# Optimization experiments

Hardware: AMD Instinct MI355X
Metric: run time of the kernel (lower is better)

Reference implementation:

```python
import jax, jax.numpy as jnp
import numpy as np
from math import pi as PI

N = 50000       # nodes
E = 625000      # edges
G = 64          # graphs in batch
H = 128         # hidden_channels
FLT = 128       # num_filters
NG = 50         # num_gaussians
L = 6           # num_layers
CUTOFF = 10.0
LOG2 = float(np.log(2.0))


def ssp(x):
    # ShiftedSoftplus
    return jax.nn.softplus(x) - LOG2


def setup_inputs() -> dict:
    key = jax.random.key(0)
    ks = jax.random.split(key, 20)
    xav = lambda k, shp: jax.random.normal(k, shp, jnp.float32) * jnp.sqrt(2.0 / (shp[-2] + shp[-1]))
    inp = {
        "z": jax.random.randint(ks[0], (N,), 0, 100),
        "pos": jax.random.normal(ks[1], (N, 3), jnp.float32),
        "batch": jnp.sort(jax.random.randint(ks[2], (N,), 0, G)),
        "edge_index": jax.random.randint(ks[3], (2, E), 0, N),
        "emb_table": jax.random.normal(ks[4], (100, H), jnp.float32),
        # per-layer stacked params, Linear stored as (in, out)
        "lin_W": xav(ks[5], (L, H, FLT)),
        "mlp_W1": xav(ks[6], (L, NG, FLT)),
        "mlp_b1": jnp.zeros((L, FLT), jnp.float32),
        "mlp_W2": xav(ks[7], (L, FLT, FLT)),
        "mlp_b2": jnp.zeros((L, FLT), jnp.float32),
        "v_W1": xav(ks[8], (L, FLT, H)),
        "v_b1": jnp.zeros((L, H), jnp.float32),
        "v_W2": xav(ks[9], (L, H, H)),
        "v_b2": jnp.zeros((L, H), jnp.float32),
        "u_W1": xav(ks[10], (H, H // 2)),
        "u_b1": jnp.zeros((H // 2,), jnp.float32),
        "u_W2": xav(ks[11], (H // 2, 1)),
        "u_b2": jnp.zeros((1,), jnp.float32),
    }
    return inp


def reference(z, pos, batch, edge_index, emb_table, lin_W, mlp_W1, mlp_b1,
              mlp_W2, mlp_b2, v_W1, v_b1, v_W2, v_b2, u_W1, u_b1, u_W2, u_b2):
    row, col = edge_index[0], edge_index[1]  # (j, i)
    dist = jnp.linalg.norm(pos[row] - pos[col], axis=-1)  # [E]

    # gaussian distance embedding
    offset = jnp.linspace(0.0, CUTOFF, NG)
    coeff = -0.5 / (offset[1] - offset[0]) ** 2
    dist_emb = jnp.exp(coeff * (dist[:, None] - offset[None, :]) ** 2)  # [E, NG]

    # cosine cutoff
    C = 0.5 * (jnp.cos(dist * (PI / CUTOFF)) + 1.0)  # [E]

    v = emb_table[z]  # [N, H]
    for l in range(L):
        # update_e
        W = ssp(dist_emb @ mlp_W1[l] + mlp_b1[l]) @ mlp_W2[l] + mlp_b2[l]
        W = W * C[:, None]                       # [E, F]
        e = (v @ lin_W[l])[row] * W              # gather v[j], filter multiply
        # update_v
        agg = jax.ops.segment_sum(e, col, num_segments=N)  # scatter-add to i
        out = ssp(agg @ v_W1[l] + v_b1[l]) @ v_W2[l] + v_b2[l]
        v = v + out

    # update_u readout
    h = ssp(v @ u_W1 + u_b1) @ u_W2 + u_b2       # [N, 1]
    u = jax.ops.segment_sum(h, batch, num_segments=G)  # [G, 1]
    return u
```

## Files before the change

kernel.cpp:

```cpp
#include <hip/hip_runtime.h>
#include <math.h>

#define H 128
#define NG 50
#define TB 2048
#define DMAX 12.0f
#define LOG2F_ 0.69314718055994531f

typedef __attribute__((ext_vector_type(8))) short bfrag8;
typedef __attribute__((ext_vector_type(4))) float f32x4;
typedef __attribute__((ext_vector_type(8))) unsigned short u16x8;

__device__ __forceinline__ float sspf(float x) {
    float xc = fminf(x, 60.f);
    float r = __logf(1.f + __expf(xc)) - LOG2F_;
    return r + fmaxf(x - 60.f, 0.f);
}
__device__ __forceinline__ float bf2f(unsigned short u) {
    union { unsigned int i; float f; } c; c.i = ((unsigned int)u) << 16; return c.f;
}
__device__ __forceinline__ unsigned short f2bf(float f) {
    union { float f; unsigned int i; } c; c.f = f;
    unsigned int r = c.i + 0x7fffu + ((c.i >> 16) & 1u);
    return (unsigned short)(r >> 16);
}

__global__ void prep_w_kernel(const float* __restrict__ linW, const float* __restrict__ vW1,
                              const float* __restrict__ vW2, unsigned short* __restrict__ Wt) {
    int mat = blockIdx.x >> 4;
    int local = (blockIdx.x & 15) * 256 + threadIdx.x;
    int nrow = local >> 5;
    int k4 = local & 31;
    const float* src = (mat < 6) ? linW + mat * 16384
                     : (mat < 12) ? vW1 + (mat - 6) * 16384
                                  : vW2 + (mat - 12) * 16384;
    ushort4 o;
    o.x = f2bf(src[(k4 * 4 + 0) * H + nrow]);
    o.y = f2bf(src[(k4 * 4 + 1) * H + nrow]);
    o.z = f2bf(src[(k4 * 4 + 2) * H + nrow]);
    o.w = f2bf(src[(k4 * 4 + 3) * H + nrow]);
    *(ushort4*)(Wt + mat * 16384 + nrow * H + k4 * 4) = o;
}

__global__ void prep_u_kernel(const float* __restrict__ uW1, unsigned short* __restrict__ Ut) {
    int idx = blockIdx.x * 256 + threadIdx.x;
    int c = idx >> 7, k = idx & 127;
    Ut[c * H + k] = f2bf(uW1[k * 64 + c]);
}

__global__ void edge_dist_kernel(const int* __restrict__ ei, const float* __restrict__ pos,
                                 float* __restrict__ et, int* __restrict__ deg,
                                 int E_, float inv_step) {
    int e = blockIdx.x * 256 + threadIdx.x;
    if (e >= E_) return;
    int j = ei[e];
    int i = ei[E_ + e];
    float dx = pos[j*3+0] - pos[i*3+0];
    float dy = pos[j*3+1] - pos[i*3+1];
    float dz = pos[j*3+2] - pos[i*3+2];
    float d = sqrtf(dx*dx + dy*dy + dz*dz);
    float t = d * inv_step;
    t = fminf(t, (float)(TB - 2) + 0.9999f);
    et[e] = t;
    atomicAdd(&deg[i], 1);
}

__global__ void hist_pb_kernel(const int* __restrict__ deg, int* __restrict__ bhist,
                               int* __restrict__ lrank, int n, int nb) {
    __shared__ int h[64];
    const int tid = threadIdx.x;
    if (tid < 64) h[tid] = 0;
    __syncthreads();
    int i = blockIdx.x * 256 + tid;
    if (i < n) lrank[i] = atomicAdd(&h[min(deg[i], 63)], 1);
    __syncthreads();
    if (tid < 64) bhist[tid * nb + blockIdx.x] = h[tid];
}

__global__ void scanb_kernel(int* __restrict__ bhist, int* __restrict__ base, int nb) {
    const int b = threadIdx.x;
    int run = 0;
    for (int k0 = 0; k0 < nb; k0 += 8) {
        int v[8];
        #pragma unroll
        for (int u = 0; u < 8; ++u)
            v[u] = (k0 + u < nb) ? bhist[b * nb + k0 + u] : 0;
        #pragma unroll
        for (int u = 0; u < 8; ++u) {
            int t = v[u];
            if (k0 + u < nb) bhist[b * nb + k0 + u] = run;
            run += t;
        }
    }
    int incl = run;
    #pragma unroll
    for (int off = 1; off < 64; off <<= 1) {
        int y = __shfl_up(incl, off, 64);
        if (b >= off) incl += y;
    }
    int total = __shfl(incl, 63, 64);
    base[b] = total - incl;
}

__global__ void place_kernel(const int* __restrict__ deg, const int* __restrict__ bhist,
                             const int* __restrict__ base, const int* __restrict__ lrank,
                             int* __restrict__ perm, int* __restrict__ iperm,
                             int* __restrict__ sdeg, int n, int nb) {
    int i = blockIdx.x * 256 + threadIdx.x;
    if (i >= n) return;
    int d = deg[i];
    int b = min(d, 63);
    int pos = base[b] + bhist[b * nb + blockIdx.x] + lrank[i];
    perm[pos] = i;
    iperm[i] = pos;
    sdeg[pos] = d;
}

__global__ void scanA_kernel(const int* __restrict__ sdeg, int* __restrict__ bsum, int n) {
    __shared__ int ws[16];
    int tid = threadIdx.x;
    int idx = blockIdx.x * 1024 + tid;
    int x = (idx < n) ? sdeg[idx] : 0;
    #pragma unroll
    for (int off = 32; off > 0; off >>= 1) x += __shfl_xor(x, off, 64);
    int lane = tid & 63, wid = tid >> 6;
    if (lane == 0) ws[wid] = x;
    __syncthreads();
    if (tid == 0) {
        int s = 0;
        #pragma unroll
        for (int i = 0; i < 16; ++i) s += ws[i];
        bsum[blockIdx.x] = s;
    }
}

__global__ void scanC_kernel(const int* __restrict__ sdeg, const int* __restrict__ bsum,
                             int* __restrict__ row_ptr, int* __restrict__ cursor, int n) {
    __shared__ int wsum[16];
    __shared__ int boff_s;
    int tid = threadIdx.x;
    int idx = blockIdx.x * 1024 + tid;
    int lane = tid & 63, wid = tid >> 6;
    if (tid == 0) {
        int s = 0;
        for (int b = 0; b < (int)blockIdx.x; ++b) s += bsum[b];
        boff_s = s;
    }
    int x = (idx < n) ? sdeg[idx] : 0;
    int v = x;
    #pragma unroll
    for (int off = 1; off < 64; off <<= 1) {
        int y = __shfl_up(v, off, 64);
        if (lane >= off) v += y;
    }
    if (lane == 63) wsum[wid] = v;
    __syncthreads();
    int woff = 0;
    for (int w = 0; w < wid; ++w) woff += wsum[w];
    int excl = boff_s + woff + v - x;
    if (idx < n) { row_ptr[idx] = excl; cursor[idx] = excl; }
    if (idx == n - 1) row_ptr[n] = excl + x;
}

__global__ void csr_fill_kernel(const int* __restrict__ ei, const float* __restrict__ et,
                                const int* __restrict__ iperm,
                                int* __restrict__ cursor, int* __restrict__ esrc,
                                float* __restrict__ et2, int E_) {
    int e = blockIdx.x * 256 + threadIdx.x;
    if (e >= E_) return;
    int pi = iperm[ei[E_ + e]];
    int slot = atomicAdd(&cursor[pi], 1);
    esrc[slot] = iperm[ei[e]];
    et2[slot] = et[e];
}

__global__ __launch_bounds__(256) void table_all_kernel(
        const float* __restrict__ mW1, const float* __restrict__ mb1,
        const float* __restrict__ mW2, const float* __restrict__ mb2,
        unsigned short* __restrict__ tbl, float step) {
    __shared__ float gs[32][52];
    __shared__ float h1s[32][132];
    const int l = blockIdx.x >> 6;
    const int r0 = (blockIdx.x & 63) * 32;
    const float* W1 = mW1 + l * NG * H;
    const float* b1 = mb1 + l * H;
    const float* W2 = mW2 + l * H * H;
    const float* b2 = mb2 + l * H;
    const int tid = threadIdx.x;
    const float offstep = 10.0f / 49.0f;
    const float coeff = -0.5f / (offstep * offstep);

    for (int idx = tid; idx < 32 * NG; idx += 256) {
        int r = idx / NG, q = idx - r * NG;
        float dd = (r0 + r) * step - q * offstep;
        gs[r][q] = __expf(coeff * dd * dd);
    }
    __syncthreads();

    const int c = tid & 127, rb = (tid >> 7) * 16;
    {
        float acc[16];
        float bv = b1[c];
        #pragma unroll
        for (int r = 0; r < 16; ++r) acc[r] = bv;
        for (int q = 0; q < NG; ++q) {
            float w = W1[q * H + c];
            #pragma unroll
            for (int r = 0; r < 16; ++r) acc[r] = fmaf(gs[rb + r][q], w, acc[r]);
        }
        #pragma unroll
        for (int r = 0; r < 16; ++r) h1s[rb + r][c] = sspf(acc[r]);
    }
    __syncthreads();
    {
        float acc[16];
        float bv = b2[c];
        #pragma unroll
        for (int r = 0; r < 16; ++r) acc[r] = bv;
        for (int f4 = 0; f4 < 32; ++f4) {
            float w0 = W2[(f4 * 4 + 0) * H + c];
            float w1 = W2[(f4 * 4 + 1) * H + c];
            float w2 = W2[(f4 * 4 + 2) * H + c];
            float w3 = W2[(f4 * 4 + 3) * H + c];
            #pragma unroll
            for (int r = 0; r < 16; ++r) {
                float4 h = *(const float4*)&h1s[rb + r][f4 * 4];
                acc[r] = fmaf(h.x, w0, acc[r]);
                acc[r] = fmaf(h.y, w1, acc[r]);
                acc[r] = fmaf(h.z, w2, acc[r]);
                acc[r] = fmaf(h.w, w3, acc[r]);
            }
        }
        #pragma unroll
        for (int r = 0; r < 16; ++r) {
            float d = (r0 + rb + r) * step;
            float C = 0.5f * (cosf(d * 0.31415926535897932f) + 1.0f);
            tbl[(size_t)l * TB * H + (size_t)(r0 + rb + r) * H + c] = f2bf(acc[r] * C);
        }
    }
}

__global__ __launch_bounds__(256) void gemm_rs_embed_kernel(
        const int* __restrict__ z, const int* __restrict__ perm,
        const float* __restrict__ emb, const unsigned short* __restrict__ Wt,
        unsigned short* __restrict__ vbf, unsigned short* __restrict__ outB, int n) {
    __shared__ unsigned short t1s[4 * 16 * H];
    const int tid = threadIdx.x;
    const int task = blockIdx.x * 4 + (tid >> 6);
    const int lane = tid & 63, l16 = lane & 15, quad = lane >> 4;
    char* t1w = (char*)(t1s + (tid >> 6) * (16 * H));
    const size_t r0 = (size_t)task * 16;
    const int p = (int)r0 + l16;
    if (p >= n) return;

    const float* erow = emb + (size_t)z[perm[p]] * H;
    bfrag8 af[4];
    #pragma unroll
    for (int kc = 0; kc < 4; ++kc) {
        const int c0 = (kc * 4 + quad) * 8;
        float4 a = *(const float4*)(erow + c0);
        float4 b = *(const float4*)(erow + c0 + 4);
        u16x8 o;
        o[0] = f2bf(a.x); o[1] = f2bf(a.y); o[2] = f2bf(a.z); o[3] = f2bf(a.w);
        o[4] = f2bf(b.x); o[5] = f2bf(b.y); o[6] = f2bf(b.z); o[7] = f2bf(b.w);
        *(u16x8*)(vbf + (size_t)p * H + c0) = o;
        af[kc] = (bfrag8)o;
    }

    #pragma unroll
    for (int ch = 0; ch < 2; ++ch) {
        bfrag8 bf[4][4];
        f32x4 acc[4];
        #pragma unroll
        for (int nt = 0; nt < 4; ++nt) {
            #pragma unroll
            for (int kc = 0; kc < 4; ++kc)
                bf[nt][kc] = *(const bfrag8*)(Wt + (size_t)(ch * 64 + nt * 16 + l16) * H
                                              + (kc * 4 + quad) * 8);
            acc[nt] = (f32x4){0.f, 0.f, 0.f, 0.f};
        }
        #pragma unroll
        for (int nt = 0; nt < 4; ++nt)
            #pragma unroll
            for (int kc = 0; kc < 4; ++kc)
                acc[nt] = __builtin_amdgcn_mfma_f32_16x16x32_bf16(af[kc], bf[nt][kc],
                                                                  acc[nt], 0, 0, 0);
        #pragma unroll
        for (int nt = 0; nt < 4; ++nt) {
            const int col = ch * 64 + nt * 16 + l16;
            const int chunk = col >> 3;
            #pragma unroll
            for (int reg = 0; reg < 4; ++reg) {
                int m = quad * 4 + reg;
                *(unsigned short*)(t1w + m * 256 + ((chunk ^ m) * 16) + (col & 7) * 2)
                    = f2bf(acc[nt][reg]);
            }
        }
    }
    asm volatile("s_waitcnt lgkmcnt(0)" ::: "memory");
    {
        const int m = lane >> 2, cg = lane & 3;
        const size_t gr = r0 + m;
        #pragma unroll
        for (int c4 = 0; c4 < 4; ++c4) {
            int chunk = cg * 4 + c4;
            u16x8 d8 = *(const u16x8*)(t1w + m * 256 + ((chunk ^ m) * 16));
            *(u16x8*)(outB + gr * H + cg * 32 + c4 * 8) = d8;
        }
    }
}

__global__ __launch_bounds__(256, 4) void layer_kernel(
        const int* __restrict__ row_ptr, const int* __restrict__ esrc,
        const float* __restrict__ et, const unsigned short* __restrict__ tbl,
        const unsigned short* __restrict__ vlin,
        const unsigned short* __restrict__ W1t, const unsigned short* __restrict__ W2t,
        const unsigned short* __restrict__ W3t,
        const float* __restrict__ b1, const float* __restrict__ b2,
        unsigned short* __restrict__ vbf, unsigned short* __restrict__ outNext, int n) {
    __shared__ unsigned short bufA[16 * H];
    __shared__ unsigned short bufB[16 * H];
    const int tid = threadIdx.x;
    const int w = tid >> 6, lane = tid & 63;
    const int r0 = blockIdx.x * 16;
    const int l16 = lane & 15, quad = lane >> 4;

    const int rrow = tid >> 4, rcolg = tid & 15;
    const int rnode = r0 + rrow;
    u16x8 rv = {0,0,0,0,0,0,0,0};
    if (rnode < n) rv = *(const u16x8*)(vbf + (size_t)rnode * H + rcolg * 8);

    {
        const int nd = w * 4 + (lane >> 4);
        const int sub = lane & 15;
        const int node = r0 + nd;
        float acc[8] = {0.f, 0.f, 0.f, 0.f, 0.f, 0.f, 0.f, 0.f};
        if (node < n) {
            const int s = row_ptr[node], e_end = row_ptr[node + 1];
            int k = s;
            for (; k + 4 <= e_end; k += 4) {
                u16x8 w0[4], w1[4], vj[4];
                float fr[4];
                #pragma unroll
                for (int e = 0; e < 4; ++e) {
                    int j = esrc[k + e];
                    float t = et[k + e];
                    int i0 = (int)t;
                    fr[e] = t - (float)i0;
                    w0[e] = *(const u16x8*)(tbl + (size_t)i0 * H + sub * 8);
                    w1[e] = *(const u16x8*)(tbl + (size_t)i0 * H + H + sub * 8);
                    vj[e] = *(const u16x8*)(vlin + (size_t)j * H + sub * 8);
                }
                #pragma unroll
                for (int e = 0; e < 4; ++e)
                    #pragma unroll
                    for (int c = 0; c < 8; ++c) {
                        float a = bf2f(w0[e][c]);
                        acc[c] = fmaf(bf2f(vj[e][c]), fmaf(bf2f(w1[e][c]) - a, fr[e], a), acc[c]);
                    }
            }
            for (; k < e_end; ++k) {
                int j = esrc[k];
                float t = et[k];
                int i0 = (int)t;
                float fr = t - (float)i0;
                u16x8 w0v = *(const u16x8*)(tbl + (size_t)i0 * H + sub * 8);
                u16x8 w1v = *(const u16x8*)(tbl + (size_t)i0 * H + H + sub * 8);
                u16x8 vj  = *(const u16x8*)(vlin + (size_t)j * H + sub * 8);
                #pragma unroll
                for (int c = 0; c < 8; ++c) {
                    float a = bf2f(w0v[c]);
                    acc[c] = fmaf(bf2f(vj[c]), fmaf(bf2f(w1v[c]) - a, fr, a), acc[c]);
                }
            }
        }
        u16x8 o;
        #pragma unroll
        for (int c = 0; c < 8; ++c) o[c] = f2bf(acc[c]);
        *(u16x8*)((char*)bufA + nd * 256 + ((sub ^ nd) * 16)) = o;
    }
    __syncthreads();

    {
        bfrag8 af[4];
        #pragma unroll
        for (int kc = 0; kc < 4; ++kc)
            af[kc] = *(const bfrag8*)((char*)bufA + l16 * 256 + (((kc * 4 + quad) ^ l16) * 16));
        #pragma unroll
        for (int nt2 = 0; nt2 < 2; ++nt2) {
            const int colt = w * 32 + nt2 * 16;
            bfrag8 bf[4];
            #pragma unroll
            for (int kc = 0; kc < 4; ++kc)
                bf[kc] = *(const bfrag8*)(W1t + (size_t)(colt + l16) * H + (kc * 4 + quad) * 8);
            f32x4 acc = (f32x4){0.f, 0.f, 0.f, 0.f};
            #pragma unroll
            for (int kc = 0; kc < 4; ++kc)
                acc = __builtin_amdgcn_mfma_f32_16x16x32_bf16(af[kc], bf[kc], acc, 0, 0, 0);
            const int f = colt + l16;
            const float bv = b1[f];
            const int chunk = f >> 3;
            #pragma unroll
            for (int reg = 0; reg < 4; ++reg) {
                int mr = quad * 4 + reg;
                *(unsigned short*)((char*)bufB + mr * 256 + ((chunk ^ mr) * 16) + (f & 7) * 2)
                    = f2bf(sspf(acc[reg] + bv));
            }
        }
    }
    __syncthreads();

    {
        bfrag8 af[4];
        #pragma unroll
        for (int kc = 0; kc < 4; ++kc)
            af[kc] = *(const bfrag8*)((char*)bufB + l16 * 256 + (((kc * 4 + quad) ^ l16) * 16));
        #pragma unroll
        for (int nt2 = 0; nt2 < 2; ++nt2) {
            const int colt = w * 32 + nt2 * 16;
            bfrag8 bf[4];
            #pragma unroll
            for (int kc = 0; kc < 4; ++kc)
                bf[kc] = *(const bfrag8*)(W2t + (size_t)(colt + l16) * H + (kc * 4 + quad) * 8);
            f32x4 acc = (f32x4){0.f, 0.f, 0.f, 0.f};
            #pragma unroll
            for (int kc = 0; kc < 4; ++kc)
                acc = __builtin_amdgcn_mfma_f32_16x16x32_bf16(af[kc], bf[kc], acc, 0, 0, 0);
            const int col = colt + l16;
            const float bv = b2[col];
            const int chunk = col >> 3;
            #pragma unroll
            for (int reg = 0; reg < 4; ++reg) {
                int mr = quad * 4 + reg;
                *(unsigned short*)((char*)bufA + mr * 256 + ((chunk ^ mr) * 16) + (col & 7) * 2)
                    = f2bf(acc[reg] + bv);
            }
        }
    }
    __syncthreads();

    {
        u16x8 d8 = *(const u16x8*)((char*)bufA + rrow * 256 + ((rcolg ^ rrow) * 16));
        u16x8 ob;
        #pragma unroll
        for (int c = 0; c < 8; ++c) ob[c] = f2bf(bf2f(rv[c]) + bf2f(d8[c]));
        if (rnode < n) *(u16x8*)(vbf + (size_t)rnode * H + rcolg * 8) = ob;
        *(u16x8*)((char*)bufB + rrow * 256 + ((rcolg ^ rrow) * 16)) = ob;
    }
    if (!W3t) return;
    __syncthreads();

    {
        bfrag8 af[4];
        #pragma unroll
        for (int kc = 0; kc < 4; ++kc)
            af[kc] = *(const bfrag8*)((char*)bufB + l16 * 256 + (((kc * 4 + quad) ^ l16) * 16));
        #pragma unroll
        for (int nt2 = 0; nt2 < 2; ++nt2) {
            const int colt = w * 32 + nt2 * 16;
            bfrag8 bf[4];
            #pragma unroll
            for (int kc = 0; kc < 4; ++kc)
                bf[kc] = *(const bfrag8*)(W3t + (size_t)(colt + l16) * H + (kc * 4 + quad) * 8);
            f32x4 acc = (f32x4){0.f, 0.f, 0.f, 0.f};
            #pragma unroll
            for (int kc = 0; kc < 4; ++kc)
                acc = __builtin_amdgcn_mfma_f32_16x16x32_bf16(af[kc], bf[kc], acc, 0, 0, 0);
            const int col = colt + l16;
            const int chunk = col >> 3;
            #pragma unroll
            for (int reg = 0; reg < 4; ++reg) {
                int mr = quad * 4 + reg;
                *(unsigned short*)((char*)bufA + mr * 256 + ((chunk ^ mr) * 16) + (col & 7) * 2)
                    = f2bf(acc[reg]);
            }
        }
    }
    __syncthreads();
    {
        u16x8 d8 = *(const u16x8*)((char*)bufA + rrow * 256 + ((rcolg ^ rrow) * 16));
        if (rnode < n) *(u16x8*)(outNext + (size_t)rnode * H + rcolg * 8) = d8;
    }
}

__global__ __launch_bounds__(256) void readout1_kernel(
        const unsigned short* __restrict__ vbf, const unsigned short* __restrict__ Ut,
        const float* __restrict__ b1, const float* __restrict__ W2,
        const float* __restrict__ b2, const int* __restrict__ batch,
        const int* __restrict__ perm, float* __restrict__ partial, int n) {
    __shared__ unsigned short As[64 * H];
    __shared__ unsigned short Bs[64 * H];
    __shared__ float gbin[64];
    const int tid = threadIdx.x;
    const int row0 = blockIdx.x * 64;

    #pragma unroll
    for (int it = 0; it < 4; ++it) {
        int idx = it * 256 + tid;
        int r = idx >> 4, c = idx & 15;
        int gr = row0 + r;
        float4 val = (gr < n) ? *(const float4*)(vbf + (size_t)gr * H + c * 8)
                              : make_float4(0.f, 0.f, 0.f, 0.f);
        *(float4*)((char*)As + r * 256 + ((c ^ (r & 15)) * 16)) = val;
    }
    #pragma unroll
    for (int it = 0; it < 4; ++it) {
        int idx = it * 256 + tid;
        int r = idx >> 4, c = idx & 15;
        float4 val = *(const float4*)(Ut + r * H + c * 8);
        *(float4*)((char*)Bs + r * 256 + ((c ^ (r & 15)) * 16)) = val;
    }
    if (tid < 64) gbin[tid] = 0.f;
    __syncthreads();

    const int lane = tid & 63, w = tid >> 6;
    const int l16 = lane & 15, quad = lane >> 4;
    const int rA = w * 16 + l16;

    bfrag8 af[4];
    #pragma unroll
    for (int kc = 0; kc < 4; ++kc) {
        int c = kc * 4 + quad;
        af[kc] = *(const bfrag8*)((const char*)As + rA * 256 + ((c ^ (rA & 15)) * 16));
    }
    f32x4 acc[4];
    #pragma unroll
    for (int nt = 0; nt < 4; ++nt) acc[nt] = (f32x4){0.f, 0.f, 0.f, 0.f};
    #pragma unroll
    for (int nt = 0; nt < 4; ++nt) {
        const int rB = nt * 16 + l16;
        #pragma unroll
        for (int kc = 0; kc < 4; ++kc) {
            int c = kc * 4 + quad;
            bfrag8 bfr = *(const bfrag8*)((const char*)Bs + rB * 256 + ((c ^ (rB & 15)) * 16));
            acc[nt] = __builtin_amdgcn_mfma_f32_16x16x32_bf16(af[kc], bfr, acc[nt], 0, 0, 0);
        }
    }

    const float b2v = b2[0];
    float rowsum[4];
    #pragma unroll
    for (int reg = 0; reg < 4; ++reg) {
        float s = 0.f;
        #pragma unroll
        for (int nt = 0; nt < 4; ++nt) {
            int col = nt * 16 + l16;
            s += sspf(acc[nt][reg] + b1[col]) * W2[col];
        }
        s += __shfl_xor(s, 1, 64);
        s += __shfl_xor(s, 2, 64);
        s += __shfl_xor(s, 4, 64);
        s += __shfl_xor(s, 8, 64);
        rowsum[reg] = s;
    }
    if (l16 == 0) {
        #pragma unroll
        for (int reg = 0; reg < 4; ++reg) {
            int node = row0 + w * 16 + quad * 4 + reg;
            if (node < n) atomicAdd(&gbin[batch[perm[node]]], rowsum[reg] + b2v);
        }
    }
    __syncthreads();
    if (tid < 64) partial[blockIdx.x * 64 + tid] = gbin[tid];
}

__global__ void readout2_kernel(const float* __restrict__ partial, float* __restrict__ out,
                                int nb) {
    __shared__ float red[256];
    const int tid = threadIdx.x;
    const int g = tid & 63, q = tid >> 6;
    float acc = 0.f;
    for (int b = q; b < nb; b += 4) acc += partial[b * 64 + g];
    red[tid] = acc;
    __syncthreads();
    if (tid < 64) out[tid] = red[tid] + red[tid + 64] + red[tid + 128] + red[tid + 192];
}

extern "C" void kernel_launch(void* const* d_in, const int* in_sizes, int n_in,
                              void* d_out, int out_size, void* d_ws, size_t ws_size,
                              hipStream_t stream) {
    const int*   z       = (const int*)d_in[0];
    const float* pos     = (const float*)d_in[1];
    const int*   batch   = (const int*)d_in[2];
    const int*   ei      = (const int*)d_in[3];
    const float* emb     = (const float*)d_in[4];
    const float* lin_W   = (const float*)d_in[5];
    const float* mlp_W1  = (const float*)d_in[6];
    const float* mlp_b1  = (const float*)d_in[7];
    const float* mlp_W2  = (const float*)d_in[8];
    const float* mlp_b2  = (const float*)d_in[9];
    const float* v_W1    = (const float*)d_in[10];
    const float* v_b1    = (const float*)d_in[11];
    const float* v_W2    = (const float*)d_in[12];
    const float* v_b2    = (const float*)d_in[13];
    const float* u_W1    = (const float*)d_in[14];
    const float* u_b1    = (const float*)d_in[15];
    const float* u_W2    = (const float*)d_in[16];
    const float* u_b2    = (const float*)d_in[17];
    const int n  = in_sizes[0];
    const int E_ = in_sizes[3] / 2;
    float* out = (float*)d_out;

    char* wp = (char*)d_ws;
    auto alloc = [&](size_t bytes) { char* p = wp; wp += (bytes + 255) & ~(size_t)255; return p; };
    const int GB = (n + 63) / 64;
    const int NB1K = (n + 1023) / 1024;
    const int NB256 = (n + 255) / 256;
    unsigned short* vbf     = (unsigned short*)alloc((size_t)n * H * 2);
    unsigned short* vlinA   = (unsigned short*)alloc((size_t)n * H * 2);
    unsigned short* vlinB   = (unsigned short*)alloc((size_t)n * H * 2);
    unsigned short* WtAll   = (unsigned short*)alloc((size_t)18 * H * H * 2);
    unsigned short* Ut      = (unsigned short*)alloc((size_t)64 * H * 2);
    unsigned short* tbl     = (unsigned short*)alloc((size_t)6 * TB * H * 2);
    float* et      = (float*)alloc((size_t)E_ * 4);
    float* et2     = (float*)alloc((size_t)E_ * 4);
    int*   esrc    = (int*)alloc((size_t)E_ * 4);
    int*   deg     = (int*)alloc((size_t)n * 4);
    int*   sdeg    = (int*)alloc((size_t)n * 4);
    int*   perm    = (int*)alloc((size_t)n * 4);
    int*   iperm   = (int*)alloc((size_t)n * 4);
    int*   lrank   = (int*)alloc((size_t)n * 4);
    int*   row_ptr = (int*)alloc((size_t)(n + 1) * 4);
    int*   cursor  = (int*)alloc((size_t)n * 4);
    int*   bsum    = (int*)alloc((size_t)NB1K * 4);
    int*   bhist   = (int*)alloc((size_t)64 * NB256 * 4);
    int*   base    = (int*)alloc(64 * 4);
    float* partial = (float*)alloc((size_t)GB * 64 * 4);

    const float step = DMAX / TB;
    hipMemsetAsync(deg, 0, (size_t)n * 4, stream);

    prep_w_kernel<<<288, 256, 0, stream>>>(lin_W, v_W1, v_W2, WtAll);
    prep_u_kernel<<<32, 256, 0, stream>>>(u_W1, Ut);
    table_all_kernel<<<384, 256, 0, stream>>>(mlp_W1, mlp_b1, mlp_W2, mlp_b2, tbl, step);
    edge_dist_kernel<<<(E_ + 255) / 256, 256, 0, stream>>>(ei, pos, et, deg, E_, 1.0f / step);
    hist_pb_kernel<<<NB256, 256, 0, stream>>>(deg, bhist, lrank, n, NB256);
    scanb_kernel<<<1, 64, 0, stream>>>(bhist, base, NB256);
    place_kernel<<<NB256, 256, 0, stream>>>(deg, bhist, base, lrank, perm, iperm, sdeg, n, NB256);
    scanA_kernel<<<NB1K, 1024, 0, stream>>>(sdeg, bsum, n);
    scanC_kernel<<<NB1K, 1024, 0, stream>>>(sdeg, bsum, row_ptr, cursor, n);
    csr_fill_kernel<<<(E_ + 255) / 256, 256, 0, stream>>>(ei, et, iperm, cursor, esrc, et2, E_);

    const int nchunk = (n + 15) / 16;
    const int GRS = (nchunk + 3) / 4;
    gemm_rs_embed_kernel<<<GRS, 256, 0, stream>>>(z, perm, emb, WtAll, vbf, vlinA, n);
    unsigned short* cur = vlinA;
    unsigned short* nxt = vlinB;
    for (int l = 0; l < 6; ++l) {
        const unsigned short* W3t = (l < 5) ? (WtAll + (l + 1) * H * H) : nullptr;
        layer_kernel<<<nchunk, 256, 0, stream>>>(row_ptr, esrc, et2,
                                                 tbl + (size_t)l * TB * H, cur,
                                                 WtAll + (6 + l) * H * H,
                                                 WtAll + (12 + l) * H * H, W3t,
                                                 v_b1 + l * H, v_b2 + l * H,
                                                 vbf, nxt, n);
        unsigned short* tmp = cur; cur = nxt; nxt = tmp;
    }
    readout1_kernel<<<GB, 256, 0, stream>>>(vbf, Ut, u_b1, u_W2, u_b2, batch, perm, partial, n);
    readout2_kernel<<<1, 256, 0, stream>>>(partial, out, GB);
}
```

Before: 662.8 us.

## Use nearest-bin filter table, pack edge data, fuse readout into last layer

Doubles the filter table resolution and replaces linear interpolation with a nearest-bin lookup. Each edge now loads one table row instead of two, with no interpolation FMAs. Edge source and bin index are packed into one int2 array, and the gather loop is unrolled to 8 edges to expose more outstanding loads. The readout MLP and per-graph partial sums are fused into the final layer kernel, which removes a separate launch and a reread of node features. The cost is a nearest-bin approximation in place of interpolation, a larger table to build, and a larger readout2 reduction.

```diff
diff --git a/kernel.cpp b/kernel.cpp
--- a/kernel.cpp
+++ b/kernel.cpp
@@ -3,7 +3,7 @@
 
 #define H 128
 #define NG 50
-#define TB 2048
+#define TB 4096
 #define DMAX 12.0f
 #define LOG2F_ 0.69314718055994531f
 
@@ -49,7 +49,7 @@
 }
 
 __global__ void edge_dist_kernel(const int* __restrict__ ei, const float* __restrict__ pos,
-                                 float* __restrict__ et, int* __restrict__ deg,
+                                 int* __restrict__ eint, int* __restrict__ deg,
                                  int E_, float inv_step) {
     int e = blockIdx.x * 256 + threadIdx.x;
     if (e >= E_) return;
@@ -59,9 +59,8 @@
     float dy = pos[j*3+1] - pos[i*3+1];
     float dz = pos[j*3+2] - pos[i*3+2];
     float d = sqrtf(dx*dx + dy*dy + dz*dz);
-    float t = d * inv_step;
-    t = fminf(t, (float)(TB - 2) + 0.9999f);
-    et[e] = t;
+    int ir = (int)(d * inv_step + 0.5f);
+    eint[e] = min(ir, TB - 1);
     atomicAdd(&deg[i], 1);
 }
 
@@ -162,16 +161,14 @@
     if (idx == n - 1) row_ptr[n] = excl + x;
 }
 
-__global__ void csr_fill_kernel(const int* __restrict__ ei, const float* __restrict__ et,
+__global__ void csr_fill_kernel(const int* __restrict__ ei, const int* __restrict__ eint,
                                 const int* __restrict__ iperm,
-                                int* __restrict__ cursor, int* __restrict__ esrc,
-                                float* __restrict__ et2, int E_) {
+                                int* __restrict__ cursor, int2* __restrict__ epack, int E_) {
     int e = blockIdx.x * 256 + threadIdx.x;
     if (e >= E_) return;
     int pi = iperm[ei[E_ + e]];
     int slot = atomicAdd(&cursor[pi], 1);
-    esrc[slot] = iperm[ei[e]];
-    et2[slot] = et[e];
+    epack[slot] = make_int2(iperm[ei[e]], eint[e]);
 }
 
 __global__ __launch_bounds__(256) void table_all_kernel(
@@ -180,8 +177,8 @@
         unsigned short* __restrict__ tbl, float step) {
     __shared__ float gs[32][52];
     __shared__ float h1s[32][132];
-    const int l = blockIdx.x >> 6;
-    const int r0 = (blockIdx.x & 63) * 32;
+    const int l = blockIdx.x >> 7;
+    const int r0 = (blockIdx.x & 127) * 32;
     const float* W1 = mW1 + l * NG * H;
     const float* b1 = mb1 + l * H;
     const float* W2 = mW2 + l * H * H;
@@ -311,15 +308,20 @@
 }
 
 __global__ __launch_bounds__(256, 4) void layer_kernel(
-        const int* __restrict__ row_ptr, const int* __restrict__ esrc,
-        const float* __restrict__ et, const unsigned short* __restrict__ tbl,
-        const unsigned short* __restrict__ vlin,
+        const int* __restrict__ row_ptr, const int2* __restrict__ epack,
+        const unsigned short* __restrict__ tbl, const unsigned short* __restrict__ vlin,
         const unsigned short* __restrict__ W1t, const unsigned short* __restrict__ W2t,
         const unsigned short* __restrict__ W3t,
         const float* __restrict__ b1, const float* __restrict__ b2,
-        unsigned short* __restrict__ vbf, unsigned short* __restrict__ outNext, int n) {
+        unsigned short* __restrict__ vbf, unsigned short* __restrict__ outNext,
+        const int* __restrict__ batch, const int* __restrict__ perm,
+        const unsigned short* __restrict__ Ut, const float* __restrict__ ub1,
+        const float* __restrict__ uW2, const float* __restrict__ ub2,
+        float* __restrict__ partial, int n) {
     __shared__ unsigned short bufA[16 * H];
     __shared__ unsigned short bufB[16 * H];
+    __shared__ float hsum[16];
+    __shared__ float gbin[64];
     const int tid = threadIdx.x;
     const int w = tid >> 6, lane = tid & 63;
     const int r0 = blockIdx.x * 16;
@@ -338,40 +340,29 @@
         if (node < n) {
             const int s = row_ptr[node], e_end = row_ptr[node + 1];
             int k = s;
-            for (; k + 4 <= e_end; k += 4) {
-                u16x8 w0[4], w1[4], vj[4];
-                float fr[4];
+            for (; k + 8 <= e_end; k += 8) {
+                int2 ep[8];
                 #pragma unroll
-                for (int e = 0; e < 4; ++e) {
-                    int j = esrc[k + e];
-                    float t = et[k + e];
-                    int i0 = (int)t;
-                    fr[e] = t - (float)i0;
-                    w0[e] = *(const u16x8*)(tbl + (size_t)i0 * H + sub * 8);
-                    w1[e] = *(const u16x8*)(tbl + (size_t)i0 * H + H + sub * 8);
-                    vj[e] = *(const u16x8*)(vlin + (size_t)j * H + sub * 8);
+                for (int e = 0; e < 8; ++e) ep[e] = epack[k + e];
+                u16x8 wv[8], vj[8];
+                #pragma unroll
+                for (int e = 0; e < 8; ++e) {
+                    wv[e] = *(const u16x8*)(tbl + (size_t)ep[e].y * H + sub * 8);
+                    vj[e] = *(const u16x8*)(vlin + (size_t)ep[e].x * H + sub * 8);
                 }
                 #pragma unroll
-                for (int e = 0; e < 4; ++e)
+                for (int e = 0; e < 8; ++e)
                     #pragma unroll
-                    for (int c = 0; c < 8; ++c) {
-                        float a = bf2f(w0[e][c]);
-                        acc[c] = fmaf(bf2f(vj[e][c]), fmaf(bf2f(w1[e][c]) - a, fr[e], a), acc[c]);
-                    }
+                    for (int c = 0; c < 8; ++c)
+                        acc[c] = fmaf(bf2f(vj[e][c]), bf2f(wv[e][c]), acc[c]);
             }
             for (; k < e_end; ++k) {
-                int j = esrc[k];
-                float t = et[k];
-                int i0 = (int)t;
-                float fr = t - (float)i0;
-                u16x8 w0v = *(const u16x8*)(tbl + (size_t)i0 * H + sub * 8);
-                u16x8 w1v = *(const u16x8*)(tbl + (size_t)i0 * H + H + sub * 8);
-                u16x8 vj  = *(const u16x8*)(vlin + (size_t)j * H + sub * 8);
+                int2 ep = epack[k];
+                u16x8 wv = *(const u16x8*)(tbl + (size_t)ep.y * H + sub * 8);
+                u16x8 vj = *(const u16x8*)(vlin + (size_t)ep.x * H + sub * 8);
                 #pragma unroll
-                for (int c = 0; c < 8; ++c) {
-                    float a = bf2f(w0v[c]);
-                    acc[c] = fmaf(bf2f(vj[c]), fmaf(bf2f(w1v[c]) - a, fr, a), acc[c]);
-                }
+                for (int c = 0; c < 8; ++c)
+                    acc[c] = fmaf(bf2f(vj[c]), bf2f(wv[c]), acc[c]);
             }
         }
         u16x8 o;
@@ -446,11 +437,12 @@
         for (int c = 0; c < 8; ++c) ob[c] = f2bf(bf2f(rv[c]) + bf2f(d8[c]));
         if (rnode < n) *(u16x8*)(vbf + (size_t)rnode * H + rcolg * 8) = ob;
         *(u16x8*)((char*)bufB + rrow * 256 + ((rcolg ^ rrow) * 16)) = ob;
-    }
-    if (!W3t) return;
-    __syncthreads();
-
-    {
+        if (tid < 16) hsum[tid] = 0.f;
+        if (tid < 64) gbin[tid] = 0.f;
+    }
+    __syncthreads();
+
+    if (W3t) {
         bfrag8 af[4];
         #pragma unroll
         for (int kc = 0; kc < 4; ++kc)
@@ -475,105 +467,58 @@
                     = f2bf(acc[reg]);
             }
         }
-    }
-    __syncthreads();
-    {
+        __syncthreads();
         u16x8 d8 = *(const u16x8*)((char*)bufA + rrow * 256 + ((rcolg ^ rrow) * 16));
         if (rnode < n) *(u16x8*)(outNext + (size_t)rnode * H + rcolg * 8) = d8;
-    }
-}
-
-__global__ __launch_bounds__(256) void readout1_kernel(
-        const unsigned short* __restrict__ vbf, const unsigned short* __restrict__ Ut,
-        const float* __restrict__ b1, const float* __restrict__ W2,
-        const float* __restrict__ b2, const int* __restrict__ batch,
-        const int* __restrict__ perm, float* __restrict__ partial, int n) {
-    __shared__ unsigned short As[64 * H];
-    __shared__ unsigned short Bs[64 * H];
-    __shared__ float gbin[64];
-    const int tid = threadIdx.x;
-    const int row0 = blockIdx.x * 64;
-
-    #pragma unroll
-    for (int it = 0; it < 4; ++it) {
-        int idx = it * 256 + tid;
-        int r = idx >> 4, c = idx & 15;
-        int gr = row0 + r;
-        float4 val = (gr < n) ? *(const float4*)(vbf + (size_t)gr * H + c * 8)
-                              : make_float4(0.f, 0.f, 0.f, 0.f);
-        *(float4*)((char*)As + r * 256 + ((c ^ (r & 15)) * 16)) = val;
-    }
-    #pragma unroll
-    for (int it = 0; it < 4; ++it) {
-        int idx = it * 256 + tid;
-        int r = idx >> 4, c = idx & 15;
-        float4 val = *(const float4*)(Ut + r * H + c * 8);
-        *(float4*)((char*)Bs + r * 256 + ((c ^ (r & 15)) * 16)) = val;
-    }
-    if (tid < 64) gbin[tid] = 0.f;
-    __syncthreads();
-
-    const int lane = tid & 63, w = tid >> 6;
-    const int l16 = lane & 15, quad = lane >> 4;
-    const int rA = w * 16 + l16;
-
-    bfrag8 af[4];
-    #pragma unroll
-    for (int kc = 0; kc < 4; ++kc) {
-        int c = kc * 4 + quad;
-        af[kc] = *(const bfrag8*)((const char*)As + rA * 256 + ((c ^ (rA & 15)) * 16));
-    }
-    f32x4 acc[4];
-    #pragma unroll
-    for (int nt = 0; nt < 4; ++nt) acc[nt] = (f32x4){0.f, 0.f, 0.f, 0.f};
-    #pragma unroll
-    for (int nt = 0; nt < 4; ++nt) {
-        const int rB = nt * 16 + l16;
-        #pragma unroll
-        for (int kc = 0; kc < 4; ++kc) {
-            int c = kc * 4 + quad;
-            bfrag8 bfr = *(const bfrag8*)((const char*)Bs + rB * 256 + ((c ^ (rB & 15)) * 16));
-            acc[nt] = __builtin_amdgcn_mfma_f32_16x16x32_bf16(af[kc], bfr, acc[nt], 0, 0, 0);
-        }
-    }
-
-    const float b2v = b2[0];
-    float rowsum[4];
-    #pragma unroll
-    for (int reg = 0; reg < 4; ++reg) {
-        float s = 0.f;
-        #pragma unroll
-        for (int nt = 0; nt < 4; ++nt) {
-            int col = nt * 16 + l16;
-            s += sspf(acc[nt][reg] + b1[col]) * W2[col];
-        }
-        s += __shfl_xor(s, 1, 64);
-        s += __shfl_xor(s, 2, 64);
-        s += __shfl_xor(s, 4, 64);
-        s += __shfl_xor(s, 8, 64);
-        rowsum[reg] = s;
-    }
-    if (l16 == 0) {
+    } else {
+        bfrag8 af[4];
+        #pragma unroll
+        for (int kc = 0; kc < 4; ++kc)
+            af[kc] = *(const bfrag8*)((char*)bufB + l16 * 256 + (((kc * 4 + quad) ^ l16) * 16));
+        const int colu = w * 16 + l16;
+        bfrag8 bfu[4];
+        #pragma unroll
+        for (int kc = 0; kc < 4; ++kc)
+            bfu[kc] = *(const bfrag8*)(Ut + (size_t)colu * H + (kc * 4 + quad) * 8);
+        f32x4 acc = (f32x4){0.f, 0.f, 0.f, 0.f};
+        #pragma unroll
+        for (int kc = 0; kc < 4; ++kc)
+            acc = __builtin_amdgcn_mfma_f32_16x16x32_bf16(af[kc], bfu[kc], acc, 0, 0, 0);
+        const float b1v = ub1[colu], w2v = uW2[colu];
         #pragma unroll
         for (int reg = 0; reg < 4; ++reg) {
-            int node = row0 + w * 16 + quad * 4 + reg;
-            if (node < n) atomicAdd(&gbin[batch[perm[node]]], rowsum[reg] + b2v);
-        }
-    }
-    __syncthreads();
-    if (tid < 64) partial[blockIdx.x * 64 + tid] = gbin[tid];
+            float s = sspf(acc[reg] + b1v) * w2v;
+            s += __shfl_xor(s, 1, 64);
+            s += __shfl_xor(s, 2, 64);
+            s += __shfl_xor(s, 4, 64);
+            s += __shfl_xor(s, 8, 64);
+            if (l16 == 0) atomicAdd(&hsum[quad * 4 + reg], s);
+        }
+        __syncthreads();
+        if (tid < 16) {
+            int node = r0 + tid;
+            if (node < n) atomicAdd(&gbin[batch[perm[node]]], hsum[tid] + ub2[0]);
+        }
+        __syncthreads();
+        if (tid < 64) partial[(size_t)blockIdx.x * 64 + tid] = gbin[tid];
+    }
 }
 
 __global__ void readout2_kernel(const float* __restrict__ partial, float* __restrict__ out,
                                 int nb) {
-    __shared__ float red[256];
+    __shared__ float red[1024];
     const int tid = threadIdx.x;
     const int g = tid & 63, q = tid >> 6;
     float acc = 0.f;
-    for (int b = q; b < nb; b += 4) acc += partial[b * 64 + g];
+    for (int b = q; b < nb; b += 16) acc += partial[(size_t)b * 64 + g];
     red[tid] = acc;
     __syncthreads();
-    if (tid < 64) out[tid] = red[tid] + red[tid + 64] + red[tid + 128] + red[tid + 192];
+    if (tid < 64) {
+        float s = 0.f;
+        #pragma unroll
+        for (int k = 0; k < 16; ++k) s += red[k * 64 + tid];
+        out[tid] = s;
+    }
 }
 
 extern "C" void kernel_launch(void* const* d_in, const int* in_sizes, int n_in,
@@ -603,18 +548,17 @@
 
     char* wp = (char*)d_ws;
     auto alloc = [&](size_t bytes) { char* p = wp; wp += (bytes + 255) & ~(size_t)255; return p; };
-    const int GB = (n + 63) / 64;
     const int NB1K = (n + 1023) / 1024;
     const int NB256 = (n + 255) / 256;
+    const int nchunk = (n + 15) / 16;
     unsigned short* vbf     = (unsigned short*)alloc((size_t)n * H * 2);
     unsigned short* vlinA   = (unsigned short*)alloc((size_t)n * H * 2);
     unsigned short* vlinB   = (unsigned short*)alloc((size_t)n * H * 2);
     unsigned short* WtAll   = (unsigned short*)alloc((size_t)18 * H * H * 2);
     unsigned short* Ut      = (unsigned short*)alloc((size_t)64 * H * 2);
     unsigned short* tbl     = (unsigned short*)alloc((size_t)6 * TB * H * 2);
-    float* et      = (float*)alloc((size_t)E_ * 4);
-    float* et2     = (float*)alloc((size_t)E_ * 4);
-    int*   esrc    = (int*)alloc((size_t)E_ * 4);
+    int*   eint    = (int*)alloc((size_t)E_ * 4);
+    int2*  epack   = (int2*)alloc((size_t)E_ * 8);
     int*   deg     = (int*)alloc((size_t)n * 4);
     int*   sdeg    = (int*)alloc((size_t)n * 4);
     int*   perm    = (int*)alloc((size_t)n * 4);
@@ -625,37 +569,37 @@
     int*   bsum    = (int*)alloc((size_t)NB1K * 4);
     int*   bhist   = (int*)alloc((size_t)64 * NB256 * 4);
     int*   base    = (int*)alloc(64 * 4);
-    float* partial = (float*)alloc((size_t)GB * 64 * 4);
+    float* partial = (float*)alloc((size_t)nchunk * 64 * 4);
 
     const float step = DMAX / TB;
     hipMemsetAsync(deg, 0, (size_t)n * 4, stream);
 
     prep_w_kernel<<<288, 256, 0, stream>>>(lin_W, v_W1, v_W2, WtAll);
     prep_u_kernel<<<32, 256, 0, stream>>>(u_W1, Ut);
-    table_all_kernel<<<384, 256, 0, stream>>>(mlp_W1, mlp_b1, mlp_W2, mlp_b2, tbl, step);
-    edge_dist_kernel<<<(E_ + 255) / 256, 256, 0, stream>>>(ei, pos, et, deg, E_, 1.0f / step);
+    table_all_kernel<<<768, 256, 0, stream>>>(mlp_W1, mlp_b1, mlp_W2, mlp_b2, tbl, step);
+    edge_dist_kernel<<<(E_ + 255) / 256, 256, 0, stream>>>(ei, pos, eint, deg, E_, 1.0f / step);
     hist_pb_kernel<<<NB256, 256, 0, stream>>>(deg, bhist, lrank, n, NB256);
     scanb_kernel<<<1, 64, 0, stream>>>(bhist, base, NB256);
     place_kernel<<<NB256, 256, 0, stream>>>(deg, bhist, base, lrank, perm, iperm, sdeg, n, NB256);
     scanA_kernel<<<NB1K, 1024, 0, stream>>>(sdeg, bsum, n);
     scanC_kernel<<<NB1K, 1024, 0, stream>>>(sdeg, bsum, row_ptr, cursor, n);
-    csr_fill_kernel<<<(E_ + 255) / 256, 256, 0, stream>>>(ei, et, iperm, cursor, esrc, et2, E_);
-
-    const int nchunk = (n + 15) / 16;
+    csr_fill_kernel<<<(E_ + 255) / 256, 256, 0, stream>>>(ei, eint, iperm, cursor, epack, E_);
+
     const int GRS = (nchunk + 3) / 4;
     gemm_rs_embed_kernel<<<GRS, 256, 0, stream>>>(z, perm, emb, WtAll, vbf, vlinA, n);
     unsigned short* cur = vlinA;
     unsigned short* nxt = vlinB;
     for (int l = 0; l < 6; ++l) {
         const unsigned short* W3t = (l < 5) ? (WtAll + (l + 1) * H * H) : nullptr;
-        layer_kernel<<<nchunk, 256, 0, stream>>>(row_ptr, esrc, et2,
+        layer_kernel<<<nchunk, 256, 0, stream>>>(row_ptr, epack,
                                                  tbl + (size_t)l * TB * H, cur,
                                                  WtAll + (6 + l) * H * H,
                                                  WtAll + (12 + l) * H * H, W3t,
                                                  v_b1 + l * H, v_b2 + l * H,
-                                                 vbf, nxt, n);
+                                                 vbf, nxt,
+                                                 batch, perm, Ut, u_b1, u_W2, u_b2,
+                                                 partial, n);
         unsigned short* tmp = cur; cur = nxt; nxt = tmp;
     }
-    readout1_kernel<<<GB, 256, 0, stream>>>(vbf, Ut, u_b1, u_W2, u_b2, batch, perm, partial, n);
-    readout2_kernel<<<1, 256, 0, stream>>>(partial, out, GB);
-}
+    readout2_kernel<<<1, 1024, 0, stream>>>(partial, out, nchunk);
+}
```

Result: slower. 680.9 us (+2.7%).
